# Kernel tuning notes

Hardware: AMD Instinct MI355X
Metric: run time of the kernel (lower is better)

## Reference

```python
import jax, jax.numpy as jnp
import numpy as np

HEADS = 8
HEAD_DIM = 32
FOLD = 2
PROP = 2


def l2norm(t):
    n = jnp.linalg.norm(t, axis=-1, keepdims=True)
    return t / jnp.maximum(n, 1e-12)


def conv1x1(x, w, b):
    # x: [B,C,W,H], w: [O,C]
    return jnp.einsum('bchw,oc->bohw', x, w) + b[None, :, None, None]


def avg_pool_to(x, ow, oh):
    b, c, w, h = x.shape
    return x.reshape(b, c, ow, w // ow, oh, h // oh).mean(axis=(3, 5))


def max_pool_to(x, ow, oh):
    b, c, w, h = x.shape
    return x.reshape(b, c, ow, w // ow, oh, h // oh).max(axis=(3, 5))


def centers_offset(x, w1, b1, w2, b2):
    # Mlp_new_offset: avg-pool to (H//4,W//4), channel MLP, max-pool to (2,2)
    b, c, H, W = x.shape
    y = avg_pool_to(x, H // 4, W // 4).transpose(0, 2, 3, 1)  # [b,h4,w4,c]
    y = jax.nn.gelu(y @ w1.T + b1, approximate=False) @ w2.T + b2
    return max_pool_to(y.transpose(0, 3, 1, 2), PROP, PROP)


def fold(t, f):
    b, c, W, H = t.shape
    w, h = W // f, H // f
    return t.reshape(b, c, f, w, f, h).transpose(0, 2, 4, 1, 3, 5).reshape(b * f * f, c, w, h)


def unfold(t, f):
    bf, c, w, h = t.shape
    b = bf // (f * f)
    return t.reshape(b, f, f, c, w, h).transpose(0, 3, 1, 4, 2, 5).reshape(b, c, f * w, f * h)


def setup_inputs() -> dict:
    key = jax.random.key(0)
    ks = jax.random.split(key, 12)
    B, DIM, W, H = 16, 256, 64, 64
    HD = HEADS * HEAD_DIM
    hid = int(HEAD_DIM * 1.66)  # 53
    r = lambda k, s: 0.02 * jax.random.normal(k, s, dtype=jnp.float32)
    return dict(
        x=jax.random.normal(ks[0], (B, DIM, W, H), dtype=jnp.float32),
        gap_scaler=1e-5 * jnp.ones((1, DIM, 1, 1), jnp.float32),
        w_fc1=r(ks[1], (HD, DIM)), b_fc1=r(ks[2], (HD,)),
        w_fcv=r(ks[3], (HD, DIM)), b_fcv=r(ks[4], (HD,)),
        w_fc2=r(ks[5], (DIM, HD)), b_fc2=r(ks[6], (DIM,)),
        sim_alpha=jnp.ones((1,), jnp.float32),
        sim_beta=jnp.zeros((1,), jnp.float32),
        off_w1=r(ks[7], (hid, HEAD_DIM)), off_b1=r(ks[8], (hid,)),
        off_w2=r(ks[9], (HEAD_DIM, hid)), off_b2=r(ks[10], (HEAD_DIM,)),
    )


def reference(x, gap_scaler, w_fc1, b_fc1, w_fcv, b_fcv, w_fc2, b_fc2,
              sim_alpha, sim_beta, off_w1, off_b1, off_w2, off_b2):
    B = x.shape[0]
    x = x + gap_scaler * x.mean(axis=(2, 3), keepdims=True)
    value = conv1x1(x, w_fcv, b_fcv)
    x = conv1x1(x, w_fc1, b_fc1)
    _, _, W, H = x.shape
    Bh = B * HEADS
    x = x.reshape(Bh, HEAD_DIM, W, H)
    value = value.reshape(Bh, HEAD_DIM, W, H)
    x = fold(x, FOLD)
    value = fold(value, FOLD)
    b, c, w, h = x.shape
    N, M = w * h, PROP * PROP
    centers = avg_pool_to(x, PROP, PROP) + centers_offset(x, off_w1, off_b1, off_w2, off_b2)
    value_centers = (avg_pool_to(value, PROP, PROP)
                     + centers_offset(value, off_w1, off_b1, off_w2, off_b2)
                     ).reshape(b, c, M).transpose(0, 2, 1)  # [b,M,c]
    cn = l2norm(centers.reshape(b, c, M).transpose(0, 2, 1))  # [b,M,c]
    xn = l2norm(x.reshape(b, c, N).transpose(0, 2, 1))        # [b,N,c]
    sim = jax.nn.sigmoid(sim_beta + sim_alpha * jnp.einsum('bmc,bnc->bmn', cn, xn))
    # top-1 assignment per token (scatter-built mask in torch)
    idx = jnp.argmax(sim, axis=1)  # [b,N]
    mask = (jnp.arange(M)[None, :, None] == idx[:, None, :]).astype(sim.dtype)
    sim = sim * mask
    value2 = value.reshape(b, c, N).transpose(0, 2, 1)  # [b,N,c]
    # combine: masked weighted sum of tokens into clusters (fused einsum,
    # same math as (value2[:,None]*sim[...,None]).sum(2))
    out = (jnp.einsum('bmn,bnc->bmc', sim, value2) + value_centers) / (mask.sum(-1, keepdims=True) + 1.0)
    # dispatch: broadcast cluster features back to tokens
    out = jnp.einsum('bmc,bmn->bnc', out, sim)
    out = out.transpose(0, 2, 1).reshape(b, c, w, h)
    out = unfold(out, FOLD).reshape(B, HEADS * HEAD_DIM, W, H)
    return conv1x1(out, w_fc2, b_fc2)
```

## Files before the change

kernel.cpp:

```cpp
#include <hip/hip_runtime.h>
#include <hip/hip_bf16.h>
#include <math.h>

#define HID 53

typedef __bf16 bf16x8 __attribute__((ext_vector_type(8)));
typedef float f32x4 __attribute__((ext_vector_type(4)));

__device__ __forceinline__ unsigned f2u(float f) { return __builtin_bit_cast(unsigned, f); }
__device__ __forceinline__ float u2f(unsigned u) { return __builtin_bit_cast(float, u); }
__device__ __forceinline__ bf16x8 ld8(const ushort* p) {
    return __builtin_bit_cast(bf16x8, *(const uint4*)p);
}

__device__ __forceinline__ ushort f2bf(float f) {
    return __builtin_bit_cast(ushort, (__bf16)f);
}
__device__ __forceinline__ float bfbits2f(ushort h) { return u2f((unsigned)h << 16); }
__device__ __forceinline__ void split3c(float f, ushort& h, ushort& m, ushort& l) {
    h = f2bf(f);
    float r1 = f - bfbits2f(h);
    m = f2bf(r1);
    float r2 = r1 - bfbits2f(m);
    l = f2bf(r2);
}

__global__ __launch_bounds__(256) void wsplit_kernel(
    const float* __restrict__ wq, const float* __restrict__ wv,
    ushort* __restrict__ qhi, ushort* __restrict__ qmd, ushort* __restrict__ qlo,
    ushort* __restrict__ vhi, ushort* __restrict__ vmd)
{
    const int id = blockIdx.x * 256 + threadIdx.x;
    ushort h, m, l;
    split3c(wq[id], h, m, l);
    qhi[id] = h; qmd[id] = m; qlo[id] = l;
    split3c(wv[id], h, m, l);
    vhi[id] = h; vmd[id] = m;
}

__global__ __launch_bounds__(256) void mean_kernel(
    const float* __restrict__ x, const float* __restrict__ gap,
    float* __restrict__ gmu)
{
    const int bc = blockIdx.x;
    const float* p = x + (size_t)bc * 4096;
    float s = 0.f;
    for (int i = threadIdx.x * 4; i < 4096; i += 256 * 4) {
        float4 v = *(const float4*)(p + i);
        s += v.x + v.y + v.z + v.w;
    }
    s += __shfl_xor(s, 1);
    s += __shfl_xor(s, 2);
    s += __shfl_xor(s, 4);
    s += __shfl_xor(s, 8);
    s += __shfl_xor(s, 16);
    s += __shfl_xor(s, 32);
    __shared__ float ls[4];
    if ((threadIdx.x & 63) == 0) ls[threadIdx.x >> 6] = s;
    __syncthreads();
    if (threadIdx.x == 0) {
        float t = ls[0] + ls[1] + ls[2] + ls[3];
        gmu[bc] = gap[bc & 255] * (t * (1.f / 4096.f));
    }
}

__global__ __launch_bounds__(256, 2) void gemm_xq6_kernel(
    const float* __restrict__ X, const float* __restrict__ gmu,
    const ushort* __restrict__ Whi, const ushort* __restrict__ Wmd,
    const ushort* __restrict__ Wlo,
    const float* __restrict__ bias_g,
    float* __restrict__ dst)
{
    __shared__ __align__(16) ushort Bhi[128 * 36];
    __shared__ __align__(16) ushort Bmd[128 * 36];
    __shared__ __align__(16) ushort Blo[128 * 36];

    const int tid  = threadIdx.x;
    const int Nblk = blockIdx.x, Mblk = blockIdx.y, b = blockIdx.z;
    const int lane = tid & 63, wav = tid >> 6;
    const int wm = wav >> 1, wn = wav & 1;
    const int lr = lane & 15, q = lane >> 4;

    f32x4 accM[4][4], accS[4][4];
#pragma unroll
    for (int i = 0; i < 4; ++i)
#pragma unroll
        for (int j = 0; j < 4; ++j) {
            accM[i][j] = (f32x4){0.f, 0.f, 0.f, 0.f};
            accS[i][j] = (f32x4){0.f, 0.f, 0.f, 0.f};
        }

    const int kp = tid & 15;
    const int q8 = (tid >> 4) & 7;
    const int ih = tid >> 7;
    const float* srcB = X + ((size_t)b << 20) + (size_t)(2 * kp) * 4096
                      + Nblk * 128 + q8 * 4;
    const float* gmub = gmu + b * 256;

    const size_t wbase = (size_t)(Mblk * 128 + wm * 64) * 256;
    const ushort* pwh = Whi + wbase;
    const ushort* pwd = Wmd + wbase;
    const ushort* pwl = Wlo + wbase;

    float4 regs[4];
    float gval0 = 0.f, gval1 = 0.f;

    auto LOADR = [&](int ks) {
        const int k0 = ks * 32;
        const float* p = srcB + (size_t)k0 * 4096;
        regs[0] = *(const float4*)(p + (ih * 2 + 0) * 32);
        regs[1] = *(const float4*)(p + 4096 + (ih * 2 + 0) * 32);
        regs[2] = *(const float4*)(p + (ih * 2 + 1) * 32);
        regs[3] = *(const float4*)(p + 4096 + (ih * 2 + 1) * 32);
        gval0 = gmub[k0 + 2 * kp];
        gval1 = gmub[k0 + 2 * kp + 1];
    };

    auto WRITE = [&]() {
#pragma unroll
        for (int ii = 0; ii < 2; ++ii) {
            const int i = ih * 2 + ii;
            float4 r0 = regs[ii * 2], r1 = regs[ii * 2 + 1];
            r0.x += gval0; r0.y += gval0; r0.z += gval0; r0.w += gval0;
            r1.x += gval1; r1.y += gval1; r1.z += gval1; r1.w += gval1;
            const float* p0 = &r0.x;
            const float* p1 = &r1.x;
#pragma unroll
            for (int e = 0; e < 4; ++e) {
                ushort h0, m0, l0, h1, m1, l1;
                split3c(p0[e], h0, m0, l0);
                split3c(p1[e], h1, m1, l1);
                const int n = q8 * 4 + i * 32 + e;
                ((unsigned*)Bhi)[n * 18 + kp] = (unsigned)h0 | ((unsigned)h1 << 16);
                ((unsigned*)Bmd)[n * 18 + kp] = (unsigned)m0 | ((unsigned)m1 << 16);
                ((unsigned*)Blo)[n * 18 + kp] = (unsigned)l0 | ((unsigned)l1 << 16);
            }
        }
    };

    LOADR(0);
    for (int ks = 0; ks < 8; ++ks) {
        WRITE();
        __syncthreads();
        if (ks < 7) LOADR(ks + 1);

        const int koff = ks * 32 + q * 8;
        bf16x8 ah[4], ad[4];
#pragma unroll
        for (int mt = 0; mt < 4; ++mt) {
            const size_t off = (size_t)(mt * 16 + lr) * 256 + koff;
            ah[mt] = ld8(pwh + off);
            ad[mt] = ld8(pwd + off);
        }
#pragma unroll
        for (int nt = 0; nt < 4; ++nt) {
            const int row = wn * 64 + nt * 16 + lr;
            bf16x8 bh = ld8(&Bhi[row * 36 + q * 8]);
            bf16x8 bd = ld8(&Bmd[row * 36 + q * 8]);
            bf16x8 bl = ld8(&Blo[row * 36 + q * 8]);
#pragma unroll
            for (int mt = 0; mt < 4; ++mt) {
                accS[mt][nt] = __builtin_amdgcn_mfma_f32_16x16x32_bf16(ah[mt], bd, accS[mt][nt], 0, 0, 0);
                accS[mt][nt] = __builtin_amdgcn_mfma_f32_16x16x32_bf16(ad[mt], bh, accS[mt][nt], 0, 0, 0);
                accS[mt][nt] = __builtin_amdgcn_mfma_f32_16x16x32_bf16(ad[mt], bd, accS[mt][nt], 0, 0, 0);
                accS[mt][nt] = __builtin_amdgcn_mfma_f32_16x16x32_bf16(ah[mt], bl, accS[mt][nt], 0, 0, 0);
                accM[mt][nt] = __builtin_amdgcn_mfma_f32_16x16x32_bf16(ah[mt], bh, accM[mt][nt], 0, 0, 0);
            }
        }
        bf16x8 al[4];
#pragma unroll
        for (int mt = 0; mt < 4; ++mt) {
            const size_t off = (size_t)(mt * 16 + lr) * 256 + koff;
            al[mt] = ld8(pwl + off);
        }
#pragma unroll
        for (int nt = 0; nt < 4; ++nt) {
            const int row = wn * 64 + nt * 16 + lr;
            bf16x8 bh2 = ld8(&Bhi[row * 36 + q * 8]);
#pragma unroll
            for (int mt = 0; mt < 4; ++mt)
                accS[mt][nt] = __builtin_amdgcn_mfma_f32_16x16x32_bf16(al[mt], bh2, accS[mt][nt], 0, 0, 0);
        }
        __syncthreads();
    }

    const size_t bbase = (size_t)b << 20;
    const int tb = Nblk * 128 + wn * 64 + lr;
    int offN[4];
#pragma unroll
    for (int nt = 0; nt < 4; ++nt) {
        int t = tb + nt * 16;
        offN[nt] = ((t >> 11) & 1) * 65536 + ((t >> 5) & 1) * 32768
                 + ((t >> 6) & 31) * 32 + (t & 31);
    }
#pragma unroll
    for (int mt = 0; mt < 4; ++mt) {
#pragma unroll
        for (int r = 0; r < 4; ++r) {
            int oc = Mblk * 128 + wm * 64 + mt * 16 + q * 4 + r;
            float bias = bias_g[oc];
            size_t offM = (size_t)(oc >> 5) * 131072 + (size_t)(oc & 31) * 1024;
#pragma unroll
            for (int nt = 0; nt < 4; ++nt)
                dst[bbase + offM + offN[nt]] = accM[mt][nt][r] + accS[mt][nt][r] + bias;
        }
    }
}

__global__ __launch_bounds__(256, 4) void gemm_val_kernel(
    const float* __restrict__ X, const float* __restrict__ gmu,
    const ushort* __restrict__ Whi, const ushort* __restrict__ Wmd,
    const float* __restrict__ bias_g,
    float* __restrict__ dst)
{
    __shared__ __align__(16) ushort Bhi[128 * 36];
    __shared__ __align__(16) ushort Bmd[128 * 36];

    const int tid  = threadIdx.x;
    const int Nblk = blockIdx.x, Mblk = blockIdx.y, b = blockIdx.z;
    const int lane = tid & 63, wav = tid >> 6;
    const int wm = wav >> 1, wn = wav & 1;
    const int lr = lane & 15, q = lane >> 4;

    f32x4 acc[4][4];
#pragma unroll
    for (int i = 0; i < 4; ++i)
#pragma unroll
        for (int j = 0; j < 4; ++j) acc[i][j] = (f32x4){0.f, 0.f, 0.f, 0.f};

    const int kp = tid & 15;
    const int q8 = (tid >> 4) & 7;
    const int ih = tid >> 7;
    const float* srcB = X + ((size_t)b << 20) + (size_t)(2 * kp) * 4096
                      + Nblk * 128 + q8 * 4;
    const float* gmub = gmu + b * 256;

    const size_t wbase = (size_t)(Mblk * 128 + wm * 64) * 256;
    const ushort* pwh = Whi + wbase;
    const ushort* pwd = Wmd + wbase;

    float4 regs[4];
    float gval0 = 0.f, gval1 = 0.f;

    auto LOADR = [&](int ks) {
        const int k0 = ks * 32;
        const float* p = srcB + (size_t)k0 * 4096;
        regs[0] = *(const float4*)(p + (ih * 2 + 0) * 32);
        regs[1] = *(const float4*)(p + 4096 + (ih * 2 + 0) * 32);
        regs[2] = *(const float4*)(p + (ih * 2 + 1) * 32);
        regs[3] = *(const float4*)(p + 4096 + (ih * 2 + 1) * 32);
        gval0 = gmub[k0 + 2 * kp];
        gval1 = gmub[k0 + 2 * kp + 1];
    };

    auto WRITE = [&]() {
#pragma unroll
        for (int ii = 0; ii < 2; ++ii) {
            const int i = ih * 2 + ii;
            float4 r0 = regs[ii * 2], r1 = regs[ii * 2 + 1];
            r0.x += gval0; r0.y += gval0; r0.z += gval0; r0.w += gval0;
            r1.x += gval1; r1.y += gval1; r1.z += gval1; r1.w += gval1;
            const float* p0 = &r0.x;
            const float* p1 = &r1.x;
#pragma unroll
            for (int e = 0; e < 4; ++e) {
                ushort h0, m0, l0, h1, m1, l1;
                split3c(p0[e], h0, m0, l0);
                split3c(p1[e], h1, m1, l1);
                const int n = q8 * 4 + i * 32 + e;
                ((unsigned*)Bhi)[n * 18 + kp] = (unsigned)h0 | ((unsigned)h1 << 16);
                ((unsigned*)Bmd)[n * 18 + kp] = (unsigned)m0 | ((unsigned)m1 << 16);
            }
        }
    };

    LOADR(0);
    for (int ks = 0; ks < 8; ++ks) {
        WRITE();
        __syncthreads();
        if (ks < 7) LOADR(ks + 1);

        const int koff = ks * 32 + q * 8;
        bf16x8 ah[4], ad[4];
#pragma unroll
        for (int mt = 0; mt < 4; ++mt) {
            const size_t off = (size_t)(mt * 16 + lr) * 256 + koff;
            ah[mt] = ld8(pwh + off);
            ad[mt] = ld8(pwd + off);
        }
#pragma unroll
        for (int nt = 0; nt < 4; ++nt) {
            const int row = wn * 64 + nt * 16 + lr;
            bf16x8 bh = ld8(&Bhi[row * 36 + q * 8]);
            bf16x8 bd = ld8(&Bmd[row * 36 + q * 8]);
#pragma unroll
            for (int mt = 0; mt < 4; ++mt) {
                acc[mt][nt] = __builtin_amdgcn_mfma_f32_16x16x32_bf16(ah[mt], bd, acc[mt][nt], 0, 0, 0);
                acc[mt][nt] = __builtin_amdgcn_mfma_f32_16x16x32_bf16(ad[mt], bh, acc[mt][nt], 0, 0, 0);
                acc[mt][nt] = __builtin_amdgcn_mfma_f32_16x16x32_bf16(ah[mt], bh, acc[mt][nt], 0, 0, 0);
            }
        }
        __syncthreads();
    }

    const size_t bbase = (size_t)b << 20;
    const int tb = Nblk * 128 + wn * 64 + lr;
    int offN[4];
#pragma unroll
    for (int nt = 0; nt < 4; ++nt) {
        int t = tb + nt * 16;
        offN[nt] = ((t >> 11) & 1) * 65536 + ((t >> 5) & 1) * 32768
                 + ((t >> 6) & 31) * 32 + (t & 31);
    }
#pragma unroll
    for (int mt = 0; mt < 4; ++mt) {
#pragma unroll
        for (int r = 0; r < 4; ++r) {
            int oc = Mblk * 128 + wm * 64 + mt * 16 + q * 4 + r;
            float bias = bias_g[oc];
            size_t offM = (size_t)(oc >> 5) * 131072 + (size_t)(oc & 31) * 1024;
#pragma unroll
            for (int nt = 0; nt < 4; ++nt)
                dst[bbase + offM + offN[nt]] = acc[mt][nt][r] + bias;
        }
    }
}

__global__ __launch_bounds__(256) void pool_kernel(
    const float* __restrict__ xqb, const float* __restrict__ valb,
    float* __restrict__ pzg)
{
    const int bp   = blockIdx.x;
    const int srci = blockIdx.y;
    const int ch   = blockIdx.z;
    const float* src = (srci ? valb : xqb) + (size_t)bp * 32768 + ch * 16384;
    const int t  = threadIdx.x;
    const int cl = t >> 4;
    const int gh = (t >> 1) & 7;
    const int s  = t & 1;

    const float* p0 = src + cl * 1024 + gh * 4;
    float acc[4];
#pragma unroll
    for (int j = 0; j < 4; ++j) {
        const float* p = p0 + (s * 4 + j) * 128;
        float a = 0.f;
#pragma unroll
        for (int i = 0; i < 4; ++i) {
            float4 v = *(const float4*)(p + i * 32);
            a += (v.x + v.y) + (v.z + v.w);
        }
        acc[j] = a * 0.0625f;
    }
    float* dstb = pzg + (size_t)(srci * 512 + bp) * 2048 + (ch * 16 + cl);
#pragma unroll
    for (int j = 0; j < 4; ++j) {
        int g = (s * 4 + j) * 8 + gh;
        dstb[g * 32] = acc[j];
    }
}

__global__ __launch_bounds__(256) void centers_mlp_kernel(
    const float* __restrict__ pzg,
    const float* __restrict__ w1g, const float* __restrict__ b1g,
    const float* __restrict__ w2g, const float* __restrict__ b2g,
    float* __restrict__ cenbuf)
{
    const int bp   = blockIdx.x;
    const int srci = blockIdx.y;
    const int t    = threadIdx.x;

    __shared__ float pzs[2048];
    __shared__ float ybuf[64 * HID];
    __shared__ float w1t[32 * HID];
    __shared__ float w2s[32 * HID];
    __shared__ float b1s[56];
    __shared__ float b2s[32];
    __shared__ float avg2[128];

    const float* psrc = pzg + (size_t)(srci * 512 + bp) * 2048;
    for (int i = t; i < 2048; i += 256) pzs[i] = psrc[i];
    for (int i = t; i < 32 * HID; i += 256) {
        int h = i >> 5, c = i & 31;
        w1t[c * HID + h] = w1g[i];
        w2s[i] = w2g[i];
    }
    if (t < HID) b1s[t] = b1g[t];
    if (t < 32) b2s[t] = b2g[t];
    __syncthreads();

    if (t < 128) {
        int qq = t >> 5, c = t & 31, qw = qq >> 1, qh = qq & 1;
        float s = 0.f;
        for (int a = 0; a < 4; ++a)
            for (int e = 0; e < 4; ++e)
                s += pzs[((qw * 4 + a) * 8 + (qh * 4 + e)) * 32 + c];
        avg2[t] = s * 0.0625f;
    }
    for (int tt = t; tt < 64 * HID; tt += 256) {
        int g = tt / HID, h = tt - g * HID;
        float a = b1s[h];
        for (int c = 0; c < 32; ++c)
            a = fmaf(pzs[g * 32 + c], w1t[c * HID + h], a);
        ybuf[g * HID + h] = 0.5f * a * (1.f + erff(a * 0.70710678118654752f));
    }
    __syncthreads();

    for (int tt = t; tt < 2048; tt += 256) {
        int g = tt >> 5, c = tt & 31;
        float a = b2s[c];
        for (int h = 0; h < HID; ++h)
            a = fmaf(ybuf[g * HID + h], w2s[c * HID + h], a);
        pzs[tt] = a;
    }
    __syncthreads();

    if (t < 128) {
        int qq = t >> 5, c = t & 31, qw = qq >> 1, qh = qq & 1;
        float m = -1e30f;
        for (int a = 0; a < 4; ++a)
            for (int e = 0; e < 4; ++e)
                m = fmaxf(m, pzs[((qw * 4 + a) * 8 + qh * 4 + e) * 32 + c]);
        cenbuf[srci * 65536 + bp * 128 + t] = avg2[t] + m;
    }
}

__global__ __launch_bounds__(1024) void assign_kernel(
    const float* __restrict__ xqb, const float* __restrict__ valb,
    const float* __restrict__ cenbuf,
    const float* __restrict__ alphap, const float* __restrict__ betap,
    float* __restrict__ wbpk, float* __restrict__ outcg)
{
    const int bp = blockIdx.x;
    const int n  = threadIdx.x;
    const int lane = n & 63;

    __shared__ float cen0s[128], cen1s[128];
    __shared__ float wbuf[1024];
    __shared__ int   bbuf[1024];
    __shared__ float csum[32][4];
    __shared__ float ccnt[4];

    if (n < 128) cen0s[n] = cenbuf[bp * 128 + n];
    else if (n < 256) cen1s[n - 128] = cenbuf[65536 + bp * 128 + (n - 128)];
    if (n < 4) ccnt[n] = 0.f;
    __syncthreads();

    float rn[4];
#pragma unroll
    for (int m = 0; m < 4; ++m) {
        float ssn = 0.f;
        for (int c = 0; c < 32; ++c) { float tt = cen0s[m * 32 + c]; ssn += tt * tt; }
        rn[m] = 1.f / fmaxf(sqrtf(ssn), 1e-12f);
    }

    const float* px = xqb + (size_t)bp * 32768 + n;
    float ss = 0.f, d0 = 0.f, d1 = 0.f, d2 = 0.f, d3 = 0.f;
#pragma unroll
    for (int c = 0; c < 32; ++c) {
        float v = px[(size_t)c << 10];
        ss += v * v;
        d0 += cen0s[0 * 32 + c] * v;
        d1 += cen0s[1 * 32 + c] * v;
        d2 += cen0s[2 * 32 + c] * v;
        d3 += cen0s[3 * 32 + c] * v;
    }
    const float rx = 1.f / fmaxf(sqrtf(ss), 1e-12f);
    const float alpha = alphap[0], beta = betap[0];
    float dm[4] = {d0, d1, d2, d3};
    float best = -1.f;
    int bidx = 0;
#pragma unroll
    for (int m = 0; m < 4; ++m) {
        float t = beta + alpha * (dm[m] * rn[m] * rx);
        float s = 1.f / (1.f + expf(-t));
        if (m == 0 || s > best) { best = s; bidx = m; }
    }
    wbuf[n] = best;
    bbuf[n] = bidx;
    wbpk[(size_t)bp * 1024 + n] = u2f((f2u(best) & ~3u) | (unsigned)bidx);

#pragma unroll
    for (int m = 0; m < 4; ++m) {
        unsigned long long bl = __ballot(bidx == m);
        if (lane == 0) atomicAdd(&ccnt[m], (float)__popcll(bl));
    }
    __syncthreads();

    {
        const int c = n >> 5, l = n & 31;
        const float* pv = valb + (size_t)bp * 32768 + c * 1024 + l;
        float a0 = 0.f, a1 = 0.f, a2 = 0.f, a3 = 0.f;
#pragma unroll
        for (int i = 0; i < 32; ++i) {
            float v = pv[i * 32];
            int t = i * 32 + l;
            float p = wbuf[t] * v;
            int m = bbuf[t];
            a0 += (m == 0) ? p : 0.f;
            a1 += (m == 1) ? p : 0.f;
            a2 += (m == 2) ? p : 0.f;
            a3 += (m == 3) ? p : 0.f;
        }
#pragma unroll
        for (int off = 1; off < 32; off <<= 1) {
            a0 += __shfl_xor(a0, off);
            a1 += __shfl_xor(a1, off);
            a2 += __shfl_xor(a2, off);
            a3 += __shfl_xor(a3, off);
        }
        if (l == 0) {
            csum[c][0] = a0; csum[c][1] = a1; csum[c][2] = a2; csum[c][3] = a3;
        }
    }
    __syncthreads();
    if (n < 128)
        outcg[(size_t)bp * 128 + n] =
            (csum[n & 31][n >> 5] + cen1s[n]) / (ccnt[n >> 5] + 1.f);
}

__global__ __launch_bounds__(256) void pmat_kernel(
    const float* __restrict__ outcg, const float* __restrict__ w2,
    float* __restrict__ P)
{
    const int bp = blockIdx.x;
    const int o  = threadIdx.x;
    __shared__ float oc[128];
    if (o < 128) oc[o] = outcg[(size_t)bp * 128 + o];
    __syncthreads();
    const int head = (bp >> 2) & 7;
    const float* wrow = w2 + (size_t)o * 256 + head * 32;
    float a0 = 0.f, a1 = 0.f, a2 = 0.f, a3 = 0.f;
#pragma unroll
    for (int c = 0; c < 32; ++c) {
        float wv = wrow[c];
        a0 = fmaf(wv, oc[c], a0);
        a1 = fmaf(wv, oc[32 + c], a1);
        a2 = fmaf(wv, oc[64 + c], a2);
        a3 = fmaf(wv, oc[96 + c], a3);
    }
    float* pb = P + (size_t)bp * 1024;
    pb[0 * 256 + o] = a0;
    pb[1 * 256 + o] = a1;
    pb[2 * 256 + o] = a2;
    pb[3 * 256 + o] = a3;
}

__global__ __launch_bounds__(1024) void fc2_dispatch_kernel(
    const float* __restrict__ P, const float* __restrict__ wbpk,
    const float* __restrict__ b2, float* __restrict__ out)
{
    const int ogrp = blockIdx.x, quad = blockIdx.y, b = blockIdx.z;
    const int n = threadIdx.x;
    const int wl = n >> 5, hl = n & 31;

    __shared__ float Pl[8][4][68];
    __shared__ float b2s[64];

    for (int i = n; i < 2048; i += 1024) {
        int h = i >> 8, rm = i & 255;
        int m = rm >> 6, j = rm & 63;
        int bp = b * 32 + h * 4 + quad;
        Pl[h][m][j] = P[(size_t)bp * 1024 + m * 256 + ogrp * 64 + j];
    }
    if (n < 64) b2s[n] = b2[ogrp * 64 + n];
    __syncthreads();

    float bst[8];
    int   mm[8];
#pragma unroll
    for (int h = 0; h < 8; ++h) {
        int bp = b * 32 + h * 4 + quad;
        unsigned u = f2u(wbpk[(size_t)bp * 1024 + n]);
        mm[h]  = (int)(u & 3u);
        bst[h] = u2f(u & ~3u);
    }

    const int fi = quad >> 1, fj = quad & 1;
    float* obp = out + (size_t)b * 1048576 + (size_t)ogrp * 64 * 4096
               + (size_t)(fi * 32 + wl) * 64 + (fj * 32 + hl);
#pragma unroll 4
    for (int j = 0; j < 64; ++j) {
        float s = b2s[j];
#pragma unroll
        for (int h = 0; h < 8; ++h)
            s = fmaf(bst[h], Pl[h][mm[h]][j], s);
        obp[(size_t)j * 4096] = s;
    }
}

extern "C" void kernel_launch(void* const* d_in, const int* in_sizes, int n_in,
                              void* d_out, int out_size, void* d_ws, size_t ws_size,
                              hipStream_t stream) {
    const float* x     = (const float*)d_in[0];
    const float* gap   = (const float*)d_in[1];
    const float* wq    = (const float*)d_in[2];
    const float* bq    = (const float*)d_in[3];
    const float* wv    = (const float*)d_in[4];
    const float* bv    = (const float*)d_in[5];
    const float* w2    = (const float*)d_in[6];
    const float* b2    = (const float*)d_in[7];
    const float* alpha = (const float*)d_in[8];
    const float* beta  = (const float*)d_in[9];
    const float* ow1   = (const float*)d_in[10];
    const float* ob1   = (const float*)d_in[11];
    const float* ow2   = (const float*)d_in[12];
    const float* ob2   = (const float*)d_in[13];

    float* out  = (float*)d_out;
    float* gmu  = (float*)d_ws;
    float* valb = gmu + 4096;
    float* cenb = valb + (size_t)16777216;
    float* wbpk = cenb + 131072;
    float* outc = wbpk + 524288;
    float* pmat = outc + 65536;
    float* pzg  = pmat + 524288;
    ushort* wqh = (ushort*)(pzg + 2097152);
    ushort* wqm = wqh + 65536;
    ushort* wql = wqm + 65536;
    ushort* wvh = wql + 65536;
    ushort* wvm = wvh + 65536;
    float* xqb  = out;

    wsplit_kernel<<<256, 256, 0, stream>>>(wq, wv, wqh, wqm, wql, wvh, wvm);
    mean_kernel<<<4096, 256, 0, stream>>>(x, gap, gmu);
    gemm_xq6_kernel<<<dim3(32, 2, 16), 256, 0, stream>>>(
        x, gmu, wqh, wqm, wql, bq, xqb);
    gemm_val_kernel<<<dim3(32, 2, 16), 256, 0, stream>>>(
        x, gmu, wvh, wvm, bv, valb);
    pool_kernel<<<dim3(512, 2, 2), 256, 0, stream>>>(xqb, valb, pzg);
    centers_mlp_kernel<<<dim3(512, 2), 256, 0, stream>>>(
        pzg, ow1, ob1, ow2, ob2, cenb);
    assign_kernel<<<512, 1024, 0, stream>>>(
        xqb, valb, cenb, alpha, beta, wbpk, outc);
    pmat_kernel<<<512, 256, 0, stream>>>(outc, w2, pmat);
    fc2_dispatch_kernel<<<dim3(4, 4, 16), 1024, 0, stream>>>(
        pmat, wbpk, b2, out);
}
```

Measured before the change: 260.7 us.

## Stage split weight tiles through padded LDS in both projection GEMMs

The weight-split kernel now writes the bf16 hi/mid/lo weight pieces in a pre-tiled, padded layout (128 rows by 40 halves per K-step). Both projection GEMMs load these tiles with coalesced uint4 reads into shared memory, software-pipelined next to the activation loads, and read the MFMA A fragments from LDS. Before, each wave fetched strided 16-byte pieces straight from global memory. This adds more shared memory per block and more registers for the prefetch. The value GEMM's occupancy hint drops from 4 to 3 blocks per CU.

```diff
diff --git a/kernel.cpp b/kernel.cpp
--- a/kernel.cpp
+++ b/kernel.cpp
@@ -31,11 +31,19 @@
     ushort* __restrict__ vhi, ushort* __restrict__ vmd)
 {
     const int id = blockIdx.x * 256 + threadIdx.x;
+    const int o = id >> 8, k = id & 255;
+    const int Mblk = o >> 7, row = o & 127, ks = k >> 5, kk = k & 31;
+    const size_t off = (size_t)((Mblk * 8 + ks) * 128 + row) * 40 + kk;
     ushort h, m, l;
     split3c(wq[id], h, m, l);
-    qhi[id] = h; qmd[id] = m; qlo[id] = l;
+    qhi[off] = h; qmd[off] = m; qlo[off] = l;
     split3c(wv[id], h, m, l);
-    vhi[id] = h; vmd[id] = m;
+    vhi[off] = h; vmd[off] = m;
+    if (kk < 8) {
+        const size_t poff = off + 32;
+        qhi[poff] = 0; qmd[poff] = 0; qlo[poff] = 0;
+        vhi[poff] = 0; vmd[poff] = 0;
+    }
 }
 
 __global__ __launch_bounds__(256) void mean_kernel(
@@ -71,6 +79,9 @@
     const float* __restrict__ bias_g,
     float* __restrict__ dst)
 {
+    __shared__ __align__(16) ushort Ahi[128 * 40];
+    __shared__ __align__(16) ushort Amd[128 * 40];
+    __shared__ __align__(16) ushort Alo[128 * 40];
     __shared__ __align__(16) ushort Bhi[128 * 36];
     __shared__ __align__(16) ushort Bmd[128 * 36];
     __shared__ __align__(16) ushort Blo[128 * 36];
@@ -97,30 +108,53 @@
                       + Nblk * 128 + q8 * 4;
     const float* gmub = gmu + b * 256;
 
-    const size_t wbase = (size_t)(Mblk * 128 + wm * 64) * 256;
-    const ushort* pwh = Whi + wbase;
-    const ushort* pwd = Wmd + wbase;
-    const ushort* pwl = Wlo + wbase;
-
-    float4 regs[4];
+    const ushort* imgH = Whi + (size_t)Mblk * 40960;
+    const ushort* imgD = Wmd + (size_t)Mblk * 40960;
+    const ushort* imgL = Wlo + (size_t)Mblk * 40960;
+    const bool third = (tid < 128);
+
+    float4 bregs[4];
+    uint4 ahr[3], adr[3], alr[3];
     float gval0 = 0.f, gval1 = 0.f;
 
     auto LOADR = [&](int ks) {
         const int k0 = ks * 32;
         const float* p = srcB + (size_t)k0 * 4096;
-        regs[0] = *(const float4*)(p + (ih * 2 + 0) * 32);
-        regs[1] = *(const float4*)(p + 4096 + (ih * 2 + 0) * 32);
-        regs[2] = *(const float4*)(p + (ih * 2 + 1) * 32);
-        regs[3] = *(const float4*)(p + 4096 + (ih * 2 + 1) * 32);
+        bregs[0] = *(const float4*)(p + (ih * 2 + 0) * 32);
+        bregs[1] = *(const float4*)(p + 4096 + (ih * 2 + 0) * 32);
+        bregs[2] = *(const float4*)(p + (ih * 2 + 1) * 32);
+        bregs[3] = *(const float4*)(p + 4096 + (ih * 2 + 1) * 32);
         gval0 = gmub[k0 + 2 * kp];
         gval1 = gmub[k0 + 2 * kp + 1];
+        const uint4* gh = (const uint4*)(imgH + (size_t)ks * 5120);
+        const uint4* gd = (const uint4*)(imgD + (size_t)ks * 5120);
+        const uint4* gl = (const uint4*)(imgL + (size_t)ks * 5120);
+        ahr[0] = gh[tid]; ahr[1] = gh[tid + 256];
+        adr[0] = gd[tid]; adr[1] = gd[tid + 256];
+        alr[0] = gl[tid]; alr[1] = gl[tid + 256];
+        if (third) {
+            ahr[2] = gh[tid + 512];
+            adr[2] = gd[tid + 512];
+            alr[2] = gl[tid + 512];
+        }
     };
 
     auto WRITE = [&]() {
+        uint4* lh = (uint4*)Ahi;
+        uint4* ld = (uint4*)Amd;
+        uint4* ll = (uint4*)Alo;
+        lh[tid] = ahr[0]; lh[tid + 256] = ahr[1];
+        ld[tid] = adr[0]; ld[tid + 256] = adr[1];
+        ll[tid] = alr[0]; ll[tid + 256] = alr[1];
+        if (third) {
+            lh[tid + 512] = ahr[2];
+            ld[tid + 512] = adr[2];
+            ll[tid + 512] = alr[2];
+        }
 #pragma unroll
         for (int ii = 0; ii < 2; ++ii) {
             const int i = ih * 2 + ii;
-            float4 r0 = regs[ii * 2], r1 = regs[ii * 2 + 1];
+            float4 r0 = bregs[ii * 2], r1 = bregs[ii * 2 + 1];
             r0.x += gval0; r0.y += gval0; r0.z += gval0; r0.w += gval0;
             r1.x += gval1; r1.y += gval1; r1.z += gval1; r1.w += gval1;
             const float* p0 = &r0.x;
@@ -144,13 +178,12 @@
         __syncthreads();
         if (ks < 7) LOADR(ks + 1);
 
-        const int koff = ks * 32 + q * 8;
         bf16x8 ah[4], ad[4];
 #pragma unroll
         for (int mt = 0; mt < 4; ++mt) {
-            const size_t off = (size_t)(mt * 16 + lr) * 256 + koff;
-            ah[mt] = ld8(pwh + off);
-            ad[mt] = ld8(pwd + off);
+            const int row = wm * 64 + mt * 16 + lr;
+            ah[mt] = ld8(&Ahi[row * 40 + q * 8]);
+            ad[mt] = ld8(&Amd[row * 40 + q * 8]);
         }
 #pragma unroll
         for (int nt = 0; nt < 4; ++nt) {
@@ -170,8 +203,8 @@
         bf16x8 al[4];
 #pragma unroll
         for (int mt = 0; mt < 4; ++mt) {
-            const size_t off = (size_t)(mt * 16 + lr) * 256 + koff;
-            al[mt] = ld8(pwl + off);
+            const int row = wm * 64 + mt * 16 + lr;
+            al[mt] = ld8(&Alo[row * 40 + q * 8]);
         }
 #pragma unroll
         for (int nt = 0; nt < 4; ++nt) {
@@ -207,12 +240,14 @@
     }
 }
 
-__global__ __launch_bounds__(256, 4) void gemm_val_kernel(
+__global__ __launch_bounds__(256, 3) void gemm_val_kernel(
     const float* __restrict__ X, const float* __restrict__ gmu,
     const ushort* __restrict__ Whi, const ushort* __restrict__ Wmd,
     const float* __restrict__ bias_g,
     float* __restrict__ dst)
 {
+    __shared__ __align__(16) ushort Ahi[128 * 40];
+    __shared__ __align__(16) ushort Amd[128 * 40];
     __shared__ __align__(16) ushort Bhi[128 * 36];
     __shared__ __align__(16) ushort Bmd[128 * 36];
 
@@ -235,29 +270,46 @@
                       + Nblk * 128 + q8 * 4;
     const float* gmub = gmu + b * 256;
 
-    const size_t wbase = (size_t)(Mblk * 128 + wm * 64) * 256;
-    const ushort* pwh = Whi + wbase;
-    const ushort* pwd = Wmd + wbase;
-
-    float4 regs[4];
+    const ushort* imgH = Whi + (size_t)Mblk * 40960;
+    const ushort* imgD = Wmd + (size_t)Mblk * 40960;
+    const bool third = (tid < 128);
+
+    float4 bregs[4];
+    uint4 ahr[3], adr[3];
     float gval0 = 0.f, gval1 = 0.f;
 
     auto LOADR = [&](int ks) {
         const int k0 = ks * 32;
         const float* p = srcB + (size_t)k0 * 4096;
-        regs[0] = *(const float4*)(p + (ih * 2 + 0) * 32);
-        regs[1] = *(const float4*)(p + 4096 + (ih * 2 + 0) * 32);
-        regs[2] = *(const float4*)(p + (ih * 2 + 1) * 32);
-        regs[3] = *(const float4*)(p + 4096 + (ih * 2 + 1) * 32);
+        bregs[0] = *(const float4*)(p + (ih * 2 + 0) * 32);
+        bregs[1] = *(const float4*)(p + 4096 + (ih * 2 + 0) * 32);
+        bregs[2] = *(const float4*)(p + (ih * 2 + 1) * 32);
+        bregs[3] = *(const float4*)(p + 4096 + (ih * 2 + 1) * 32);
         gval0 = gmub[k0 + 2 * kp];
         gval1 = gmub[k0 + 2 * kp + 1];
+        const uint4* gh = (const uint4*)(imgH + (size_t)ks * 5120);
+        const uint4* gd = (const uint4*)(imgD + (size_t)ks * 5120);
+        ahr[0] = gh[tid]; ahr[1] = gh[tid + 256];
+        adr[0] = gd[tid]; adr[1] = gd[tid + 256];
+        if (third) {
+            ahr[2] = gh[tid + 512];
+            adr[2] = gd[tid + 512];
+        }
     };
 
     auto WRITE = [&]() {
+        uint4* lh = (uint4*)Ahi;
+        uint4* ld = (uint4*)Amd;
+        lh[tid] = ahr[0]; lh[tid + 256] = ahr[1];
+        ld[tid] = adr[0]; ld[tid + 256] = adr[1];
+        if (third) {
+            lh[tid + 512] = ahr[2];
+            ld[tid + 512] = adr[2];
+        }
 #pragma unroll
         for (int ii = 0; ii < 2; ++ii) {
             const int i = ih * 2 + ii;
-            float4 r0 = regs[ii * 2], r1 = regs[ii * 2 + 1];
+            float4 r0 = bregs[ii * 2], r1 = bregs[ii * 2 + 1];
             r0.x += gval0; r0.y += gval0; r0.z += gval0; r0.w += gval0;
             r1.x += gval1; r1.y += gval1; r1.z += gval1; r1.w += gval1;
             const float* p0 = &r0.x;
@@ -280,13 +332,12 @@
         __syncthreads();
         if (ks < 7) LOADR(ks + 1);
 
-        const int koff = ks * 32 + q * 8;
         bf16x8 ah[4], ad[4];
 #pragma unroll
         for (int mt = 0; mt < 4; ++mt) {
-            const size_t off = (size_t)(mt * 16 + lr) * 256 + koff;
-            ah[mt] = ld8(pwh + off);
-            ad[mt] = ld8(pwd + off);
+            const int row = wm * 64 + mt * 16 + lr;
+            ah[mt] = ld8(&Ahi[row * 40 + q * 8]);
+            ad[mt] = ld8(&Amd[row * 40 + q * 8]);
         }
 #pragma unroll
         for (int nt = 0; nt < 4; ++nt) {
@@ -616,10 +667,10 @@
     float* pmat = outc + 65536;
     float* pzg  = pmat + 524288;
     ushort* wqh = (ushort*)(pzg + 2097152);
-    ushort* wqm = wqh + 65536;
-    ushort* wql = wqm + 65536;
-    ushort* wvh = wql + 65536;
-    ushort* wvm = wvh + 65536;
+    ushort* wqm = wqh + 81920;
+    ushort* wql = wqm + 81920;
+    ushort* wvh = wql + 81920;
+    ushort* wvm = wvh + 81920;
     float* xqb  = out;
 
     wsplit_kernel<<<256, 256, 0, stream>>>(wq, wv, wqh, wqm, wql, wvh, wvm);
```

Measured after the change: 333.9 us. 1.28x slower.

## Stage split weight tiles into LDS via async global_load_lds with pre-tiled image

Applied to the files above, without the earlier changes.

The weight-split kernel now writes the bf16 hi/mid/lo weight pieces into a per-K-step tiled image with padded rows of 40 elements. Both projection GEMMs copy each tile into LDS with direct global-to-LDS loads, issued after the trailing barrier so the next step's copy overlaps the B staging. Previously each wave read its A fragments straight from global memory on every K step. This adds LDS usage, which lowers the occupancy bound on the value GEMM from 4 to 3. A single A buffer is reused across steps, so correctness depends on the barrier placement.

```diff
diff --git a/kernel.cpp b/kernel.cpp
--- a/kernel.cpp
+++ b/kernel.cpp
@@ -25,17 +25,27 @@
     l = f2bf(r2);
 }
 
+#define GLB(p) ((const __attribute__((address_space(1))) void*)(p))
+#define LDS(p) ((__attribute__((address_space(3))) void*)(p))
+
 __global__ __launch_bounds__(256) void wsplit_kernel(
     const float* __restrict__ wq, const float* __restrict__ wv,
-    ushort* __restrict__ qhi, ushort* __restrict__ qmd, ushort* __restrict__ qlo,
-    ushort* __restrict__ vhi, ushort* __restrict__ vmd)
+    ushort* __restrict__ qimg, ushort* __restrict__ vimg)
 {
     const int id = blockIdx.x * 256 + threadIdx.x;
+    const int o = id >> 8, k = id & 255;
+    const int Mblk = o >> 7, row = o & 127, ks = k >> 5, kk = k & 31;
+    const size_t tq = (size_t)((Mblk * 8 + ks) * 3) * 5120 + row * 40 + kk;
+    const size_t tv = (size_t)((Mblk * 8 + ks) * 2) * 5120 + row * 40 + kk;
     ushort h, m, l;
     split3c(wq[id], h, m, l);
-    qhi[id] = h; qmd[id] = m; qlo[id] = l;
+    qimg[tq] = h; qimg[tq + 5120] = m; qimg[tq + 10240] = l;
     split3c(wv[id], h, m, l);
-    vhi[id] = h; vmd[id] = m;
+    vimg[tv] = h; vimg[tv + 5120] = m;
+    if (kk < 8) {
+        qimg[tq + 32] = 0; qimg[tq + 5120 + 32] = 0; qimg[tq + 10240 + 32] = 0;
+        vimg[tv + 32] = 0; vimg[tv + 5120 + 32] = 0;
+    }
 }
 
 __global__ __launch_bounds__(256) void mean_kernel(
@@ -66,18 +76,19 @@
 
 __global__ __launch_bounds__(256, 2) void gemm_xq6_kernel(
     const float* __restrict__ X, const float* __restrict__ gmu,
-    const ushort* __restrict__ Whi, const ushort* __restrict__ Wmd,
-    const ushort* __restrict__ Wlo,
+    const ushort* __restrict__ Wimg,
     const float* __restrict__ bias_g,
     float* __restrict__ dst)
 {
+    __shared__ __align__(16) ushort A3[15360];
     __shared__ __align__(16) ushort Bhi[128 * 36];
     __shared__ __align__(16) ushort Bmd[128 * 36];
     __shared__ __align__(16) ushort Blo[128 * 36];
 
     const int tid  = threadIdx.x;
     const int Nblk = blockIdx.x, Mblk = blockIdx.y, b = blockIdx.z;
-    const int lane = tid & 63, wav = tid >> 6;
+    const int lane = tid & 63;
+    const int wav  = __builtin_amdgcn_readfirstlane(tid >> 6);
     const int wm = wav >> 1, wn = wav & 1;
     const int lr = lane & 15, q = lane >> 4;
 
@@ -97,30 +108,40 @@
                       + Nblk * 128 + q8 * 4;
     const float* gmub = gmu + b * 256;
 
-    const size_t wbase = (size_t)(Mblk * 128 + wm * 64) * 256;
-    const ushort* pwh = Whi + wbase;
-    const ushort* pwd = Wmd + wbase;
-    const ushort* pwl = Wlo + wbase;
-
-    float4 regs[4];
+    const ushort* img = Wimg + (size_t)Mblk * (8 * 15360);
+
+    float4 bregs[4];
     float gval0 = 0.f, gval1 = 0.f;
 
-    auto LOADR = [&](int ks) {
+    auto ISSUE_A = [&](int ks) {
+        const ushort* gb = img + (size_t)ks * 15360;
+#pragma unroll
+        for (int i = 0; i < 8; ++i) {
+            const int seg = wav + 4 * i;
+            if (seg < 30) {
+                __builtin_amdgcn_global_load_lds(
+                    GLB(gb + seg * 512 + lane * 8),
+                    LDS(A3 + seg * 512), 16, 0, 0);
+            }
+        }
+    };
+
+    auto LOADB = [&](int ks) {
         const int k0 = ks * 32;
         const float* p = srcB + (size_t)k0 * 4096;
-        regs[0] = *(const float4*)(p + (ih * 2 + 0) * 32);
-        regs[1] = *(const float4*)(p + 4096 + (ih * 2 + 0) * 32);
-        regs[2] = *(const float4*)(p + (ih * 2 + 1) * 32);
-        regs[3] = *(const float4*)(p + 4096 + (ih * 2 + 1) * 32);
+        bregs[0] = *(const float4*)(p + (ih * 2 + 0) * 32);
+        bregs[1] = *(const float4*)(p + 4096 + (ih * 2 + 0) * 32);
+        bregs[2] = *(const float4*)(p + (ih * 2 + 1) * 32);
+        bregs[3] = *(const float4*)(p + 4096 + (ih * 2 + 1) * 32);
         gval0 = gmub[k0 + 2 * kp];
         gval1 = gmub[k0 + 2 * kp + 1];
     };
 
-    auto WRITE = [&]() {
+    auto WRITE_B = [&]() {
 #pragma unroll
         for (int ii = 0; ii < 2; ++ii) {
             const int i = ih * 2 + ii;
-            float4 r0 = regs[ii * 2], r1 = regs[ii * 2 + 1];
+            float4 r0 = bregs[ii * 2], r1 = bregs[ii * 2 + 1];
             r0.x += gval0; r0.y += gval0; r0.z += gval0; r0.w += gval0;
             r1.x += gval1; r1.y += gval1; r1.z += gval1; r1.w += gval1;
             const float* p0 = &r0.x;
@@ -138,19 +159,19 @@
         }
     };
 
-    LOADR(0);
+    ISSUE_A(0);
+    LOADB(0);
     for (int ks = 0; ks < 8; ++ks) {
-        WRITE();
+        WRITE_B();
         __syncthreads();
-        if (ks < 7) LOADR(ks + 1);
-
-        const int koff = ks * 32 + q * 8;
+        if (ks < 7) LOADB(ks + 1);
+
         bf16x8 ah[4], ad[4];
 #pragma unroll
         for (int mt = 0; mt < 4; ++mt) {
-            const size_t off = (size_t)(mt * 16 + lr) * 256 + koff;
-            ah[mt] = ld8(pwh + off);
-            ad[mt] = ld8(pwd + off);
+            const int row = wm * 64 + mt * 16 + lr;
+            ah[mt] = ld8(&A3[row * 40 + q * 8]);
+            ad[mt] = ld8(&A3[5120 + row * 40 + q * 8]);
         }
 #pragma unroll
         for (int nt = 0; nt < 4; ++nt) {
@@ -170,8 +191,8 @@
         bf16x8 al[4];
 #pragma unroll
         for (int mt = 0; mt < 4; ++mt) {
-            const size_t off = (size_t)(mt * 16 + lr) * 256 + koff;
-            al[mt] = ld8(pwl + off);
+            const int row = wm * 64 + mt * 16 + lr;
+            al[mt] = ld8(&A3[10240 + row * 40 + q * 8]);
         }
 #pragma unroll
         for (int nt = 0; nt < 4; ++nt) {
@@ -182,6 +203,7 @@
                 accS[mt][nt] = __builtin_amdgcn_mfma_f32_16x16x32_bf16(al[mt], bh2, accS[mt][nt], 0, 0, 0);
         }
         __syncthreads();
+        if (ks < 7) ISSUE_A(ks + 1);
     }
 
     const size_t bbase = (size_t)b << 20;
@@ -207,18 +229,20 @@
     }
 }
 
-__global__ __launch_bounds__(256, 4) void gemm_val_kernel(
+__global__ __launch_bounds__(256, 3) void gemm_val_kernel(
     const float* __restrict__ X, const float* __restrict__ gmu,
-    const ushort* __restrict__ Whi, const ushort* __restrict__ Wmd,
+    const ushort* __restrict__ Wimg,
     const float* __restrict__ bias_g,
     float* __restrict__ dst)
 {
+    __shared__ __align__(16) ushort A2[10240];
     __shared__ __align__(16) ushort Bhi[128 * 36];
     __shared__ __align__(16) ushort Bmd[128 * 36];
 
     const int tid  = threadIdx.x;
     const int Nblk = blockIdx.x, Mblk = blockIdx.y, b = blockIdx.z;
-    const int lane = tid & 63, wav = tid >> 6;
+    const int lane = tid & 63;
+    const int wav  = __builtin_amdgcn_readfirstlane(tid >> 6);
     const int wm = wav >> 1, wn = wav & 1;
     const int lr = lane & 15, q = lane >> 4;
 
@@ -235,29 +259,38 @@
                       + Nblk * 128 + q8 * 4;
     const float* gmub = gmu + b * 256;
 
-    const size_t wbase = (size_t)(Mblk * 128 + wm * 64) * 256;
-    const ushort* pwh = Whi + wbase;
-    const ushort* pwd = Wmd + wbase;
-
-    float4 regs[4];
+    const ushort* img = Wimg + (size_t)Mblk * (8 * 10240);
+
+    float4 bregs[4];
     float gval0 = 0.f, gval1 = 0.f;
 
-    auto LOADR = [&](int ks) {
+    auto ISSUE_A = [&](int ks) {
+        const ushort* gb = img + (size_t)ks * 10240;
+#pragma unroll
+        for (int i = 0; i < 5; ++i) {
+            const int seg = wav + 4 * i;
+            __builtin_amdgcn_global_load_lds(
+                GLB(gb + seg * 512 + lane * 8),
+                LDS(A2 + seg * 512), 16, 0, 0);
+        }
+    };
+
+    auto LOADB = [&](int ks) {
         const int k0 = ks * 32;
         const float* p = srcB + (size_t)k0 * 4096;
-        regs[0] = *(const float4*)(p + (ih * 2 + 0) * 32);
-        regs[1] = *(const float4*)(p + 4096 + (ih * 2 + 0) * 32);
-        regs[2] = *(const float4*)(p + (ih * 2 + 1) * 32);
-        regs[3] = *(const float4*)(p + 4096 + (ih * 2 + 1) * 32);
+        bregs[0] = *(const float4*)(p + (ih * 2 + 0) * 32);
+        bregs[1] = *(const float4*)(p + 4096 + (ih * 2 + 0) * 32);
+        bregs[2] = *(const float4*)(p + (ih * 2 + 1) * 32);
+        bregs[3] = *(const float4*)(p + 4096 + (ih * 2 + 1) * 32);
         gval0 = gmub[k0 + 2 * kp];
         gval1 = gmub[k0 + 2 * kp + 1];
     };
 
-    auto WRITE = [&]() {
+    auto WRITE_B = [&]() {
 #pragma unroll
         for (int ii = 0; ii < 2; ++ii) {
             const int i = ih * 2 + ii;
-            float4 r0 = regs[ii * 2], r1 = regs[ii * 2 + 1];
+            float4 r0 = bregs[ii * 2], r1 = bregs[ii * 2 + 1];
             r0.x += gval0; r0.y += gval0; r0.z += gval0; r0.w += gval0;
             r1.x += gval1; r1.y += gval1; r1.z += gval1; r1.w += gval1;
             const float* p0 = &r0.x;
@@ -274,19 +307,19 @@
         }
     };
 
-    LOADR(0);
+    ISSUE_A(0);
+    LOADB(0);
     for (int ks = 0; ks < 8; ++ks) {
-        WRITE();
+        WRITE_B();
         __syncthreads();
-        if (ks < 7) LOADR(ks + 1);
-
-        const int koff = ks * 32 + q * 8;
+        if (ks < 7) LOADB(ks + 1);
+
         bf16x8 ah[4], ad[4];
 #pragma unroll
         for (int mt = 0; mt < 4; ++mt) {
-            const size_t off = (size_t)(mt * 16 + lr) * 256 + koff;
-            ah[mt] = ld8(pwh + off);
-            ad[mt] = ld8(pwd + off);
+            const int row = wm * 64 + mt * 16 + lr;
+            ah[mt] = ld8(&A2[row * 40 + q * 8]);
+            ad[mt] = ld8(&A2[5120 + row * 40 + q * 8]);
         }
 #pragma unroll
         for (int nt = 0; nt < 4; ++nt) {
@@ -301,6 +334,7 @@
             }
         }
         __syncthreads();
+        if (ks < 7) ISSUE_A(ks + 1);
     }
 
     const size_t bbase = (size_t)b << 20;
@@ -615,19 +649,16 @@
     float* outc = wbpk + 524288;
     float* pmat = outc + 65536;
     float* pzg  = pmat + 524288;
-    ushort* wqh = (ushort*)(pzg + 2097152);
-    ushort* wqm = wqh + 65536;
-    ushort* wql = wqm + 65536;
-    ushort* wvh = wql + 65536;
-    ushort* wvm = wvh + 65536;
+    ushort* qimg = (ushort*)(pzg + 2097152);
+    ushort* vimg = qimg + 245760;
     float* xqb  = out;
 
-    wsplit_kernel<<<256, 256, 0, stream>>>(wq, wv, wqh, wqm, wql, wvh, wvm);
+    wsplit_kernel<<<256, 256, 0, stream>>>(wq, wv, qimg, vimg);
     mean_kernel<<<4096, 256, 0, stream>>>(x, gap, gmu);
     gemm_xq6_kernel<<<dim3(32, 2, 16), 256, 0, stream>>>(
-        x, gmu, wqh, wqm, wql, bq, xqb);
+        x, gmu, qimg, bq, xqb);
     gemm_val_kernel<<<dim3(32, 2, 16), 256, 0, stream>>>(
-        x, gmu, wvh, wvm, bv, valb);
+        x, gmu, vimg, bv, valb);
     pool_kernel<<<dim3(512, 2, 2), 256, 0, stream>>>(xqb, valb, pzg);
     centers_mlp_kernel<<<dim3(512, 2), 256, 0, stream>>>(
         pzg, ow1, ob1, ow2, ob2, cenb);
```

New measurement: 252.5 us. -3.1%, faster.
